# Kernel optimization log

Measured on AMD Instinct MI355X. Metric: run time of the kernel, lower is better.

The kernel has to match this reference:

```python
import jax, jax.numpy as jnp
import numpy as np

N_EMBD = 768
NUM_HEADS = 12
HEAD_DIM = 64
B, S = 4, 2048


def setup_inputs() -> dict:
    key = jax.random.key(0)
    ks = jax.random.split(key, 9)
    scale = 1.0 / np.sqrt(N_EMBD)
    def lin(k):
        kw, kb = jax.random.split(k)
        W = jax.random.uniform(kw, (N_EMBD, N_EMBD), jnp.float32, -scale, scale)
        b = jax.random.uniform(kb, (N_EMBD,), jnp.float32, -scale, scale)
        return W, b
    wq_w, wq_b = lin(ks[0])
    wk_w, wk_b = lin(ks[1])
    wv_w, wv_b = lin(ks[2])
    wo_w, wo_b = lin(ks[3])
    x = jax.random.normal(ks[4], (B, S, N_EMBD), jnp.float32)
    return {
        "x": x,
        "wq_w": wq_w, "wq_b": wq_b,
        "wk_w": wk_w, "wk_b": wk_b,
        "wv_w": wv_w, "wv_b": wv_b,
        "wo_w": wo_w, "wo_b": wo_b,
    }


def reference(x, wq_w, wq_b, wk_w, wk_b, wv_w, wv_b, wo_w, wo_b):
    bs, sl, dim = x.shape
    # Linear projections (torch Linear: x @ W.T + b)
    q = x @ wq_w.T + wq_b
    k = x @ wk_w.T + wk_b
    v = x @ wv_w.T + wv_b
    # [B, S, H, D] -> [B, H, S, D]
    q = q.reshape(bs, sl, NUM_HEADS, HEAD_DIM).transpose(0, 2, 1, 3)
    k = k.reshape(bs, sl, NUM_HEADS, HEAD_DIM).transpose(0, 2, 1, 3)
    v = v.reshape(bs, sl, NUM_HEADS, HEAD_DIM).transpose(0, 2, 1, 3)
    # scores: [B, H, S, S]
    attn = jnp.einsum("bhqd,bhkd->bhqk", q, k) / jnp.sqrt(jnp.float32(HEAD_DIM))
    attn = jax.nn.softmax(attn, axis=-1)
    # dropout is identity in eval mode (reference baseline)
    out = jnp.einsum("bhqk,bhkd->bhqd", attn, v)  # [B, H, S, D]
    out = out.transpose(0, 2, 1, 3).reshape(bs, sl, dim)
    return out @ wo_w.T + wo_b
```

## Files before the change

kernel.cpp:

```cpp
#include <hip/hip_runtime.h>
#include <stdint.h>
#include <stddef.h>

#define NEMBD 768
#define NH    12
#define HD    64
#define SEQ   2048
#define TOK   8192
#define QKVN  2304
#define NT    (SEQ / 64)
#define QSCALE 0.18033688011112042f

typedef __attribute__((ext_vector_type(4))) float f32x4;
typedef __attribute__((ext_vector_type(8))) __bf16 bf8;
typedef __attribute__((ext_vector_type(8))) short s16x8;
typedef __attribute__((ext_vector_type(4))) short s16x4;

static __device__ __forceinline__ short f2bf(float f) {
  __bf16 h = (__bf16)f;
  union { __bf16 h; short s; } u; u.h = h; return u.s;
}

typedef const __attribute__((address_space(1))) unsigned int* gp1;
typedef __attribute__((address_space(3))) unsigned int* lp3;
static __device__ __forceinline__ void gload_lds16(const void* g, void* l) {
  __builtin_amdgcn_global_load_lds((gp1)g, (lp3)l, 16, 0, 0);
}

__global__ __launch_bounds__(256) void prep_kern(
    const float* __restrict__ x, short* __restrict__ xb,
    const float* __restrict__ wq, const float* __restrict__ wk, const float* __restrict__ wv,
    const float* __restrict__ wo, const float* __restrict__ bq, const float* __restrict__ bk,
    const float* __restrict__ bv, short* __restrict__ wqkv, short* __restrict__ wo16,
    float* __restrict__ bqkv) {
  const int WN = NEMBD * NEMBD;
  int blk = blockIdx.x;
  if (blk < 6144) {
    int i = (blk * 256 + threadIdx.x) * 4;
    f32x4 v = *(const f32x4*)(x + i);
    s16x4 o;
#pragma unroll
    for (int j = 0; j < 4; ++j) o[j] = f2bf(v[j]);
    *(s16x4*)(xb + i) = o;
    return;
  }
  int t = (blk - 6144) * 256 + threadIdx.x;
  const int n4 = WN;
  if (t < n4) {
    int i4 = t * 4;
    const float* src; short* dst; int rem;
    if (i4 < 3 * WN) {
      int which = i4 / WN;
      rem = i4 - which * WN;
      src = which == 0 ? wq : (which == 1 ? wk : wv);
      dst = wqkv + i4;
    } else {
      rem = i4 - 3 * WN;
      src = wo;
      dst = wo16 + rem;
    }
    f32x4 v = *(const f32x4*)(src + rem);
    s16x4 o;
#pragma unroll
    for (int j = 0; j < 4; ++j) o[j] = f2bf(v[j]);
    *(s16x4*)dst = o;
  } else {
    int t2 = t - n4;
    if (t2 < QKVN) {
      int which = t2 / NEMBD, rem = t2 - which * NEMBD;
      bqkv[t2] = (which == 0 ? bq : (which == 1 ? bk : bv))[rem];
    }
  }
}

template <int EPI, int BN>
__global__ __launch_bounds__(256) void gemm128(
    const short* __restrict__ A, const short* __restrict__ Bw, const float* __restrict__ bias,
    short* __restrict__ q_out, short* __restrict__ k_out, short* __restrict__ v_out,
    float* __restrict__ c_out, int M, int N, int K) {
  __shared__ short As[128 * 64];
  __shared__ short Bs[BN * 64];
  const int NFR = BN / 32;
  const int tid = threadIdx.x;
  const int wave = tid >> 6, lane = tid & 63;
  const int r = lane & 15, g = lane >> 4;

  const int nwg = gridDim.x * gridDim.y;
  const int bid = blockIdx.y * gridDim.x + blockIdx.x;
  const int sb = (bid & 7) * (nwg >> 3) + (bid >> 3);
  const int bx = sb % gridDim.x, by = sb / gridDim.x;

  const int n0 = bx * BN, m0 = by * 128;
  const int wm0 = (wave >> 1) * 64, wn0 = (wave & 1) * (BN / 2);
  const int lrow = lane >> 3;
  const int lcol = ((lane & 7) ^ (lane >> 3)) * 8;
  const int cbr = (r & 7) << 4;

  f32x4 acc[4][NFR];
#pragma unroll
  for (int mi = 0; mi < 4; ++mi)
#pragma unroll
    for (int ni = 0; ni < NFR; ++ni) acc[mi][ni] = (f32x4){0.f, 0.f, 0.f, 0.f};

  for (int kt = 0; kt < K; kt += 64) {
#pragma unroll
    for (int ii = 0; ii < 4; ++ii) {
      int blk = wave * 4 + ii;
      gload_lds16(A + (size_t)(m0 + blk * 8 + lrow) * K + kt + lcol, &As[blk * 512]);
    }
#pragma unroll
    for (int ii = 0; ii < BN / 32; ++ii) {
      int blk = wave * (BN / 32) + ii;
      gload_lds16(Bw + (size_t)(n0 + blk * 8 + lrow) * K + kt + lcol, &Bs[blk * 512]);
    }
    __syncthreads();
#pragma unroll
    for (int kk = 0; kk < 2; ++kk) {
      int cb = (kk * 64 + g * 16) ^ cbr;
      bf8 af[4], bfv[NFR];
#pragma unroll
      for (int mi = 0; mi < 4; ++mi)
        af[mi] = *(const bf8*)((const char*)As + (wm0 + 16 * mi + r) * 128 + cb);
#pragma unroll
      for (int ni = 0; ni < NFR; ++ni)
        bfv[ni] = *(const bf8*)((const char*)Bs + (wn0 + 16 * ni + r) * 128 + cb);
#pragma unroll
      for (int mi = 0; mi < 4; ++mi)
#pragma unroll
        for (int ni = 0; ni < NFR; ++ni) {
          if (EPI == 1)
            acc[mi][ni] = __builtin_amdgcn_mfma_f32_16x16x32_bf16(af[mi], bfv[ni], acc[mi][ni], 0, 0, 0);
          else
            acc[mi][ni] = __builtin_amdgcn_mfma_f32_16x16x32_bf16(bfv[ni], af[mi], acc[mi][ni], 0, 0, 0);
        }
    }
    __syncthreads();
  }

  if (EPI == 2) {
#pragma unroll
    for (int ni = 0; ni < NFR; ++ni) {
      int colb = n0 + wn0 + 16 * ni + 4 * g;
      f32x4 bv4 = *(const f32x4*)&bias[colb];
#pragma unroll
      for (int mi = 0; mi < 4; ++mi) {
        int row = m0 + wm0 + 16 * mi + r;
        f32x4 ov;
#pragma unroll
        for (int j = 0; j < 4; ++j) ov[j] = acc[mi][ni][j] + bv4[j];
        *(f32x4*)&c_out[(size_t)row * N + colb] = ov;
      }
    }
  } else if (EPI == 0) {
#pragma unroll
    for (int ni = 0; ni < NFR; ++ni) {
      int colb = n0 + wn0 + 16 * ni + 4 * g;
      int which = colb / NEMBD;
      int rem = colb - which * NEMBD;
      int h = rem >> 6, d0 = rem & 63;
      short* dst = which == 0 ? q_out : k_out;
      float sc = which == 0 ? QSCALE : 1.0f;
      f32x4 bv4 = *(const f32x4*)&bias[colb];
#pragma unroll
      for (int mi = 0; mi < 4; ++mi) {
        int row = m0 + wm0 + 16 * mi + r;
        int b = row >> 11, s = row & 2047;
        s16x4 pk;
#pragma unroll
        for (int j = 0; j < 4; ++j) pk[j] = f2bf((acc[mi][ni][j] + bv4[j]) * sc);
        *(s16x4*)&dst[(((size_t)(b * NH + h)) * SEQ + s) * HD + d0] = pk;
      }
    }
  } else {
#pragma unroll
    for (int ni = 0; ni < NFR; ++ni) {
      int col = n0 + wn0 + 16 * ni + r;
      float bcol = bias[col];
      int h = col >> 6, d = col & 63;
#pragma unroll
      for (int mi = 0; mi < 4; ++mi) {
        int s0 = m0 + wm0 + 16 * mi + 4 * g;
        int b = s0 >> 11, s = s0 & 2047;
        s16x4 pk;
#pragma unroll
        for (int j = 0; j < 4; ++j) pk[j] = f2bf(acc[mi][ni][j] + bcol);
        *(s16x4*)&v_out[(((size_t)(b * NH + h)) * HD + d) * SEQ + s] = pk;
      }
    }
  }
}

__global__ __launch_bounds__(512) void attn_kern(
    const short* __restrict__ Qg, const short* __restrict__ Kg, const short* __restrict__ Vtg,
    short* __restrict__ Ao) {
  __shared__ short Kl[64 * 64];
  __shared__ short Vl[64 * 64];
  __shared__ short Pl[8][16 * 64];

  const int tid = threadIdx.x;
  const int wave = tid >> 6, lane = tid & 63;
  const int r = lane & 15, g = lane >> 4;

  const int nwg = gridDim.x * gridDim.y;
  const int bid = blockIdx.y * gridDim.x + blockIdx.x;
  const int sb = (bid & 7) * (nwg >> 3) + (bid >> 3);
  const int bh = sb >> 4;
  const int q0 = (sb & 15) * 128;
  const size_t base = (size_t)bh * (SEQ * HD);

  bf8 qf[2];
#pragma unroll
  for (int kk = 0; kk < 2; ++kk)
    qf[kk] = *(const bf8*)&Qg[base + (size_t)(q0 + wave * 16 + r) * HD + kk * 32 + g * 8];

  union { short s; __bf16 h; } one_u; one_u.s = 0x3F80;
  bf8 vones;
#pragma unroll
  for (int i = 0; i < 8; ++i) vones[i] = one_u.h;

  f32x4 o[4], osum;
#pragma unroll
  for (int fd = 0; fd < 4; ++fd) o[fd] = (f32x4){0.f, 0.f, 0.f, 0.f};
  osum = (f32x4){0.f, 0.f, 0.f, 0.f};

  const int cbr = (r & 7) << 4;
  short* Pw = &Pl[wave][0];

  const int srow = tid >> 3;
  const int sc8 = ((tid & 7) ^ (srow & 7)) * 8;

  for (int t = 0; t < NT; ++t) {
    gload_lds16(Kg + base + (size_t)(t * 64 + srow) * HD + sc8, &Kl[wave * 512]);
    gload_lds16(Vtg + base + (size_t)srow * SEQ + t * 64 + sc8, &Vl[wave * 512]);
    __syncthreads();

    f32x4 sv[4];
#pragma unroll
    for (int f = 0; f < 4; ++f) sv[f] = (f32x4){0.f, 0.f, 0.f, 0.f};
    __builtin_amdgcn_s_setprio(1);
#pragma unroll
    for (int kk = 0; kk < 2; ++kk) {
      int cb = (kk * 64 + g * 16) ^ cbr;
#pragma unroll
      for (int f = 0; f < 4; ++f) {
        bf8 kf = *(const bf8*)((const char*)Kl + (16 * f + r) * 128 + cb);
        sv[f] = __builtin_amdgcn_mfma_f32_16x16x32_bf16(kf, qf[kk], sv[f], 0, 0, 0);
      }
    }
    __builtin_amdgcn_s_setprio(0);

#pragma unroll
    for (int f = 0; f < 4; ++f) {
      s16x4 pk;
#pragma unroll
      for (int j = 0; j < 4; ++j)
        pk[j] = f2bf(__builtin_amdgcn_exp2f(sv[f][j]));
      *(s16x4*)((char*)Pw + r * 128 + ((32 * f + 8 * g) ^ cbr)) = pk;
    }

    __builtin_amdgcn_s_setprio(1);
#pragma unroll
    for (int kk = 0; kk < 2; ++kk) {
      bf8 pa = *(const bf8*)((const char*)Pw + r * 128 + ((64 * kk + 16 * g) ^ cbr));
      int cb = (kk * 64 + g * 16) ^ cbr;
      osum = __builtin_amdgcn_mfma_f32_16x16x32_bf16(pa, vones, osum, 0, 0, 0);
#pragma unroll
      for (int fd = 0; fd < 4; ++fd) {
        bf8 vb = *(const bf8*)((const char*)Vl + (16 * fd + r) * 128 + cb);
        o[fd] = __builtin_amdgcn_mfma_f32_16x16x32_bf16(pa, vb, o[fd], 0, 0, 0);
      }
    }
    __builtin_amdgcn_s_setprio(0);
    __syncthreads();
  }

  const int b = bh / NH, h = bh - b * NH;
#pragma unroll
  for (int j = 0; j < 4; ++j) {
    float ij = 1.f / osum[j];
    int srow_o = q0 + wave * 16 + 4 * g + j;
    size_t obase = ((size_t)(b * SEQ + srow_o)) * NEMBD + h * HD;
#pragma unroll
    for (int fd = 0; fd < 4; ++fd)
      Ao[obase + 16 * fd + r] = f2bf(o[fd][j] * ij);
  }
}

extern "C" void kernel_launch(void* const* d_in, const int* in_sizes, int n_in,
                              void* d_out, int out_size, void* d_ws, size_t ws_size,
                              hipStream_t stream) {
  (void)in_sizes; (void)n_in; (void)out_size; (void)ws_size;
  const float* x   = (const float*)d_in[0];
  const float* wqw = (const float*)d_in[1];
  const float* wqb = (const float*)d_in[2];
  const float* wkw = (const float*)d_in[3];
  const float* wkb = (const float*)d_in[4];
  const float* wvw = (const float*)d_in[5];
  const float* wvb = (const float*)d_in[6];
  const float* wow = (const float*)d_in[7];
  const float* wob = (const float*)d_in[8];

  char* ws = (char*)d_ws;
  short* xb   = (short*)(ws + 0);
  short* wqkv = (short*)(ws + 12582912);
  short* wo16 = (short*)(ws + 16121856);
  float* bqkv = (float*)(ws + 17301504);
  short* qb   = (short*)(ws + 17310720);
  short* kb   = (short*)(ws + 29893632);
  short* vb   = (short*)(ws + 42476544);

  prep_kern<<<dim3(6144 + 2313), dim3(256), 0, stream>>>(
      x, xb, wqw, wkw, wvw, wow, wqb, wkb, wvb, wqkv, wo16, bqkv);
  gemm128<0, 128><<<dim3(12, TOK / 128), dim3(256), 0, stream>>>(
      xb, wqkv, bqkv, qb, kb, nullptr, nullptr, TOK, QKVN, NEMBD);
  gemm128<1, 128><<<dim3(6, TOK / 128), dim3(256), 0, stream>>>(
      xb, wqkv + (size_t)2 * NEMBD * NEMBD, bqkv + 2 * NEMBD, nullptr, nullptr, vb,
      nullptr, TOK, QKVN, NEMBD);
  attn_kern<<<dim3(SEQ / 128, 48), dim3(512), 0, stream>>>(qb, kb, vb, xb);
  gemm128<2, 64><<<dim3(NEMBD / 64, TOK / 128), dim3(256), 0, stream>>>(
      xb, wo16, wob, nullptr, nullptr, nullptr, (float*)d_out, TOK, NEMBD, NEMBD);
}
```

Baseline: 149.0 us.

## Process two 16-row query blocks per wave in attention with 4-wave blocks

The attention kernel now uses 256 threads (4 waves) per block, and each wave handles 32 query rows as two 16-row sub-blocks instead of 16 rows. Each K and V fragment read from LDS now feeds two MFMAs, halving LDS reads per unit of work, and each thread issues twice as many global-to-LDS loads per tile. In exchange the kernel holds more registers per thread for the doubled accumulators and score tiles, and there are fewer waves per block to hide latency.

```diff
diff --git a/kernel.cpp b/kernel.cpp
--- a/kernel.cpp
+++ b/kernel.cpp
@@ -190,12 +190,12 @@
   }
 }
 
-__global__ __launch_bounds__(512) void attn_kern(
+__global__ __launch_bounds__(256) void attn_kern(
     const short* __restrict__ Qg, const short* __restrict__ Kg, const short* __restrict__ Vtg,
     short* __restrict__ Ao) {
   __shared__ short Kl[64 * 64];
   __shared__ short Vl[64 * 64];
-  __shared__ short Pl[8][16 * 64];
+  __shared__ short Pl[4][32 * 64];
 
   const int tid = threadIdx.x;
   const int wave = tid >> 6, lane = tid & 63;
@@ -208,35 +208,47 @@
   const int q0 = (sb & 15) * 128;
   const size_t base = (size_t)bh * (SEQ * HD);
 
-  bf8 qf[2];
-#pragma unroll
-  for (int kk = 0; kk < 2; ++kk)
-    qf[kk] = *(const bf8*)&Qg[base + (size_t)(q0 + wave * 16 + r) * HD + kk * 32 + g * 8];
+  bf8 qf[2][2];
+#pragma unroll
+  for (int qb = 0; qb < 2; ++qb)
+#pragma unroll
+    for (int kk = 0; kk < 2; ++kk)
+      qf[qb][kk] = *(const bf8*)&Qg[base + (size_t)(q0 + wave * 32 + qb * 16 + r) * HD +
+                                    kk * 32 + g * 8];
 
   union { short s; __bf16 h; } one_u; one_u.s = 0x3F80;
   bf8 vones;
 #pragma unroll
   for (int i = 0; i < 8; ++i) vones[i] = one_u.h;
 
-  f32x4 o[4], osum;
-#pragma unroll
-  for (int fd = 0; fd < 4; ++fd) o[fd] = (f32x4){0.f, 0.f, 0.f, 0.f};
-  osum = (f32x4){0.f, 0.f, 0.f, 0.f};
+  f32x4 o[2][4], osum[2];
+#pragma unroll
+  for (int qb = 0; qb < 2; ++qb) {
+#pragma unroll
+    for (int fd = 0; fd < 4; ++fd) o[qb][fd] = (f32x4){0.f, 0.f, 0.f, 0.f};
+    osum[qb] = (f32x4){0.f, 0.f, 0.f, 0.f};
+  }
 
   const int cbr = (r & 7) << 4;
   short* Pw = &Pl[wave][0];
 
   const int srow = tid >> 3;
   const int sc8 = ((tid & 7) ^ (srow & 7)) * 8;
+  const int srow2 = (256 + tid) >> 3;
+  const int sc82 = (((256 + tid) & 7) ^ (srow2 & 7)) * 8;
 
   for (int t = 0; t < NT; ++t) {
     gload_lds16(Kg + base + (size_t)(t * 64 + srow) * HD + sc8, &Kl[wave * 512]);
     gload_lds16(Vtg + base + (size_t)srow * SEQ + t * 64 + sc8, &Vl[wave * 512]);
+    gload_lds16(Kg + base + (size_t)(t * 64 + srow2) * HD + sc82, &Kl[2048 + wave * 512]);
+    gload_lds16(Vtg + base + (size_t)srow2 * SEQ + t * 64 + sc82, &Vl[2048 + wave * 512]);
     __syncthreads();
 
-    f32x4 sv[4];
-#pragma unroll
-    for (int f = 0; f < 4; ++f) sv[f] = (f32x4){0.f, 0.f, 0.f, 0.f};
+    f32x4 sv[2][4];
+#pragma unroll
+    for (int qb = 0; qb < 2; ++qb)
+#pragma unroll
+      for (int f = 0; f < 4; ++f) sv[qb][f] = (f32x4){0.f, 0.f, 0.f, 0.f};
     __builtin_amdgcn_s_setprio(1);
 #pragma unroll
     for (int kk = 0; kk < 2; ++kk) {
@@ -244,30 +256,36 @@
 #pragma unroll
       for (int f = 0; f < 4; ++f) {
         bf8 kf = *(const bf8*)((const char*)Kl + (16 * f + r) * 128 + cb);
-        sv[f] = __builtin_amdgcn_mfma_f32_16x16x32_bf16(kf, qf[kk], sv[f], 0, 0, 0);
+        sv[0][f] = __builtin_amdgcn_mfma_f32_16x16x32_bf16(kf, qf[0][kk], sv[0][f], 0, 0, 0);
+        sv[1][f] = __builtin_amdgcn_mfma_f32_16x16x32_bf16(kf, qf[1][kk], sv[1][f], 0, 0, 0);
       }
     }
     __builtin_amdgcn_s_setprio(0);
 
 #pragma unroll
-    for (int f = 0; f < 4; ++f) {
-      s16x4 pk;
-#pragma unroll
-      for (int j = 0; j < 4; ++j)
-        pk[j] = f2bf(__builtin_amdgcn_exp2f(sv[f][j]));
-      *(s16x4*)((char*)Pw + r * 128 + ((32 * f + 8 * g) ^ cbr)) = pk;
-    }
+    for (int qb = 0; qb < 2; ++qb)
+#pragma unroll
+      for (int f = 0; f < 4; ++f) {
+        s16x4 pk;
+#pragma unroll
+        for (int j = 0; j < 4; ++j)
+          pk[j] = f2bf(__builtin_amdgcn_exp2f(sv[qb][f][j]));
+        *(s16x4*)((char*)Pw + (qb * 16 + r) * 128 + ((32 * f + 8 * g) ^ cbr)) = pk;
+      }
 
     __builtin_amdgcn_s_setprio(1);
 #pragma unroll
     for (int kk = 0; kk < 2; ++kk) {
-      bf8 pa = *(const bf8*)((const char*)Pw + r * 128 + ((64 * kk + 16 * g) ^ cbr));
       int cb = (kk * 64 + g * 16) ^ cbr;
-      osum = __builtin_amdgcn_mfma_f32_16x16x32_bf16(pa, vones, osum, 0, 0, 0);
+      bf8 pa0 = *(const bf8*)((const char*)Pw + r * 128 + ((64 * kk + 16 * g) ^ cbr));
+      bf8 pa1 = *(const bf8*)((const char*)Pw + (16 + r) * 128 + ((64 * kk + 16 * g) ^ cbr));
+      osum[0] = __builtin_amdgcn_mfma_f32_16x16x32_bf16(pa0, vones, osum[0], 0, 0, 0);
+      osum[1] = __builtin_amdgcn_mfma_f32_16x16x32_bf16(pa1, vones, osum[1], 0, 0, 0);
 #pragma unroll
       for (int fd = 0; fd < 4; ++fd) {
         bf8 vb = *(const bf8*)((const char*)Vl + (16 * fd + r) * 128 + cb);
-        o[fd] = __builtin_amdgcn_mfma_f32_16x16x32_bf16(pa, vb, o[fd], 0, 0, 0);
+        o[0][fd] = __builtin_amdgcn_mfma_f32_16x16x32_bf16(pa0, vb, o[0][fd], 0, 0, 0);
+        o[1][fd] = __builtin_amdgcn_mfma_f32_16x16x32_bf16(pa1, vb, o[1][fd], 0, 0, 0);
       }
     }
     __builtin_amdgcn_s_setprio(0);
@@ -276,14 +294,16 @@
 
   const int b = bh / NH, h = bh - b * NH;
 #pragma unroll
-  for (int j = 0; j < 4; ++j) {
-    float ij = 1.f / osum[j];
-    int srow_o = q0 + wave * 16 + 4 * g + j;
-    size_t obase = ((size_t)(b * SEQ + srow_o)) * NEMBD + h * HD;
-#pragma unroll
-    for (int fd = 0; fd < 4; ++fd)
-      Ao[obase + 16 * fd + r] = f2bf(o[fd][j] * ij);
-  }
+  for (int qb = 0; qb < 2; ++qb)
+#pragma unroll
+    for (int j = 0; j < 4; ++j) {
+      float ij = 1.f / osum[qb][j];
+      int srow_o = q0 + wave * 32 + qb * 16 + 4 * g + j;
+      size_t obase = ((size_t)(b * SEQ + srow_o)) * NEMBD + h * HD;
+#pragma unroll
+      for (int fd = 0; fd < 4; ++fd)
+        Ao[obase + 16 * fd + r] = f2bf(o[qb][fd][j] * ij);
+    }
 }
 
 extern "C" void kernel_launch(void* const* d_in, const int* in_sizes, int n_in,
@@ -316,7 +336,7 @@
   gemm128<1, 128><<<dim3(6, TOK / 128), dim3(256), 0, stream>>>(
       xb, wqkv + (size_t)2 * NEMBD * NEMBD, bqkv + 2 * NEMBD, nullptr, nullptr, vb,
       nullptr, TOK, QKVN, NEMBD);
-  attn_kern<<<dim3(SEQ / 128, 48), dim3(512), 0, stream>>>(qb, kb, vb, xb);
+  attn_kern<<<dim3(SEQ / 128, 48), dim3(256), 0, stream>>>(qb, kb, vb, xb);
   gemm128<2, 64><<<dim3(NEMBD / 64, TOK / 128), dim3(256), 0, stream>>>(
       xb, wo16, wob, nullptr, nullptr, nullptr, (float*)d_out, TOK, NEMBD, NEMBD);
 }
```

After: 152.9 us. +2.6%, slower.
